# Performance work log

Hardware: AMD Instinct MI355X
Metric: run time of the kernel (lower is better)

Reference implementation:

```python
import jax, jax.numpy as jnp
import numpy as np

B, N, D, H = 2, 2048, 1024, 16
DH = D // H  # 64


def setup_inputs() -> dict:
    key = jax.random.key(0)
    ks = jax.random.split(key, 5)
    s = 1.0 / np.sqrt(D)
    x = jax.random.normal(ks[0], (B, N, D), jnp.float32)
    # per-head kqv Linear weights, stacked: [H, D, 3*DH]
    Wkqv = jax.random.normal(ks[1], (H, D, 3 * DH), jnp.float32) * s
    bkqv = jax.random.normal(ks[2], (H, 3 * DH), jnp.float32) * 0.02
    Wo = jax.random.normal(ks[3], (D, D), jnp.float32) * s
    bo = jax.random.normal(ks[4], (D,), jnp.float32) * 0.02
    return {"x": x, "Wkqv": Wkqv, "bkqv": bkqv, "Wo": Wo, "bo": bo}


def reference(x, Wkqv, bkqv, Wo, bo):
    Bs, Ns, Ds = x.shape
    Hs = Wkqv.shape[0]
    dh = Wkqv.shape[-1] // 3
    # all heads' kqv projections at once: [B, H, N, 3*dh]
    kqv_out = jnp.einsum('bnd,hde->bhne', x, Wkqv) + bkqv[None, :, None, :]
    # original splits in order (k, q, v)
    k, q, v = jnp.split(kqv_out, 3, axis=-1)
    # NOTE: original computes attention_scores(k, q) = k @ q^T (swapped vs standard)
    A = jnp.einsum('bhnd,bhmd->bhnm', k, q) / jnp.sqrt(jnp.asarray(dh, x.dtype))
    mask = jnp.tril(jnp.ones((Ns, Ns), dtype=bool))
    A = jnp.where(mask[None, None], A, -jnp.inf)
    alpha = jax.nn.softmax(A, axis=-1)
    sa = jnp.einsum('bhnm,bhmd->bhnd', alpha, v)  # [B, H, N, dh]
    # concat heads along feature dim (head0..headH-1 order)
    sa = sa.transpose(0, 2, 1, 3).reshape(Bs, Ns, Hs * dh)
    return sa @ Wo + bo
```

## Files before the change

### kernel.cpp

```cpp
#include <hip/hip_runtime.h>
#include <hip/hip_bf16.h>
#include <cstdint>
#include <cstddef>

typedef __bf16 bf16x8 __attribute__((ext_vector_type(8)));
typedef __bf16 bf16x4 __attribute__((ext_vector_type(4)));
typedef float  f32x4  __attribute__((ext_vector_type(4)));

constexpr int Bc = 2, Nc = 2048, Dc = 1024, Hc = 16, DHc = 64;
constexpr int BN = Bc * Nc;
constexpr int E3 = 3 * DHc;
constexpr int BH = Bc * Hc;
constexpr int NK = Hc * E3;

__device__ __forceinline__ f32x4 mfma16(bf16x8 a, bf16x8 b, f32x4 c) {
  return __builtin_amdgcn_mfma_f32_16x16x32_bf16(a, b, c, 0, 0, 0);
}

__device__ __forceinline__ void gload16(const __bf16* g, __bf16* l) {
  __builtin_amdgcn_global_load_lds((const __attribute__((address_space(1))) void*)g,
                                   (__attribute__((address_space(3))) void*)l,
                                   16, 0, 0);
}

__device__ __forceinline__ float fexp2(float x) {
  return __builtin_amdgcn_exp2f(x);
}

__global__ void cvt_x_kernel(const float* __restrict__ x, __bf16* __restrict__ xb) {
  int i = (blockIdx.x * 256 + threadIdx.x) * 4;
  float4 v = *(const float4*)(x + i);
  xb[i + 0] = (__bf16)v.x;
  xb[i + 1] = (__bf16)v.y;
  xb[i + 2] = (__bf16)v.z;
  xb[i + 3] = (__bf16)v.w;
}

constexpr int TP = 68;
__global__ void cvt_T_kernel(const float* __restrict__ src, __bf16* __restrict__ dst,
                             int R, int C) {
  __shared__ __bf16 T[64][TP];
  const int c0 = blockIdx.x * 64, r0 = blockIdx.y * 64;
  const size_t sbase = (size_t)blockIdx.z * R * C;
  const int tid = threadIdx.x;
#pragma unroll
  for (int it = 0; it < 4; ++it) {
    int g = tid + it * 256;
    int r = g >> 4, c4 = (g & 15) * 4;
    float4 v = *(const float4*)&src[sbase + (size_t)(r0 + r) * C + c0 + c4];
    T[c4 + 0][r] = (__bf16)v.x;
    T[c4 + 1][r] = (__bf16)v.y;
    T[c4 + 2][r] = (__bf16)v.z;
    T[c4 + 3][r] = (__bf16)v.w;
  }
  __syncthreads();
#pragma unroll
  for (int it = 0; it < 2; ++it) {
    int g = tid + it * 256;
    int c = g >> 3, ch = (g & 7) * 8;
    bf16x4 u0 = *(const bf16x4*)&T[c][ch];
    bf16x4 u1 = *(const bf16x4*)&T[c][ch + 4];
    __bf16* dp = &dst[sbase + (size_t)(c0 + c) * R + r0 + ch];
    *(bf16x4*)dp = u0;
    *(bf16x4*)(dp + 4) = u1;
  }
}

__launch_bounds__(256)
__global__ void kqv_gemm_kernel(const __bf16* __restrict__ xb,
                                const __bf16* __restrict__ wkt,
                                const float* __restrict__ bkqv,
                                __bf16* __restrict__ kqv,
                                __bf16* __restrict__ vT) {
  const int mt = blockIdx.x;
  const int h  = blockIdx.y;
  __shared__ __align__(16) __bf16 Al[2][128][64];
  __shared__ __align__(16) __bf16 Bl[2][192][64];
  const int tid  = threadIdx.x;
  const int lane = tid & 63;
  const int w    = tid >> 6;
  const int fr   = lane & 15, fq = lane >> 4;
  const int fq4  = fq * 4;
  const int WR   = (w >> 1) * 64, WC = (w & 1) * 96;
  const int sr   = tid >> 3;
  const int sc8  = ((tid & 7) ^ (sr & 7)) * 8;
  const int wb   = (w << 3);
  const int m0   = mt * 128;
  const __bf16* wth = wkt + (size_t)h * E3 * Dc;

  auto STAGE = [&](int buf, int k0) {
#pragma unroll
    for (int j = 0; j < 4; ++j)
      gload16(&xb[(size_t)(m0 + j * 32 + sr) * Dc + k0 + sc8], &Al[buf][j * 32 + wb][0]);
#pragma unroll
    for (int j = 0; j < 6; ++j)
      gload16(&wth[(size_t)(j * 32 + sr) * Dc + k0 + sc8], &Bl[buf][j * 32 + wb][0]);
  };

  f32x4 acc[4][6] = {};
  STAGE(0, 0);
  int cur = 0;
  for (int t = 0; t < 16; ++t) {
    if (t < 15) {
      STAGE(cur ^ 1, (t + 1) * 64);
      asm volatile("s_waitcnt vmcnt(10)" ::: "memory");
    } else {
      asm volatile("s_waitcnt vmcnt(0)" ::: "memory");
    }
    asm volatile("s_barrier" ::: "memory");
    const char* Ab = (const char*)&Al[cur][0][0];
    const char* Bb = (const char*)&Bl[cur][0][0];
#pragma unroll
    for (int ks = 0; ks < 2; ++ks) {
      bf16x8 a_[4], b_[6];
#pragma unroll
      for (int mr = 0; mr < 4; ++mr) {
        int r = WR + mr * 16 + fr;
        a_[mr] = *(const bf16x8*)(Ab + r * 128 + ((ks * 64 + fq * 16) ^ ((r & 7) << 4)));
      }
#pragma unroll
      for (int nc = 0; nc < 6; ++nc) {
        int r = WC + nc * 16 + fr;
        b_[nc] = *(const bf16x8*)(Bb + r * 128 + ((ks * 64 + fq * 16) ^ ((r & 7) << 4)));
      }
#pragma unroll
      for (int mr = 0; mr < 4; ++mr)
#pragma unroll
        for (int nc = 0; nc < 6; ++nc)
          acc[mr][nc] = mfma16(a_[mr], b_[nc], acc[mr][nc]);
    }
    asm volatile("s_barrier" ::: "memory");
    cur ^= 1;
  }

  const int b = m0 >> 11;
#pragma unroll
  for (int nc = 0; nc < 6; ++nc) {
    const int eb = WC + nc * 16;
    const float bias = bkqv[h * E3 + eb + fr];
    if (eb < 64) {
      const float sc = 0.125f * 1.44269504088896f;
      const int el = eb + fr;
#pragma unroll
      for (int mr = 0; mr < 4; ++mr) {
        int nn0 = (m0 & (Nc - 1)) + WR + mr * 16 + fq4;
        bf16x4 v4;
#pragma unroll
        for (int i = 0; i < 4; ++i) v4[i] = (__bf16)((acc[mr][nc][i] + bias) * sc);
        *(bf16x4*)&kqv[((size_t)((b * Hc + h) * DHc + el)) * Nc + nn0] = v4;
      }
    } else if (eb < 128) {
      const int e = (eb - 64) + fr;
      __bf16* dst = kqv + (size_t)BH * Nc * DHc +
                    ((size_t)(b * Hc + h)) * Nc * DHc + e;
#pragma unroll
      for (int mr = 0; mr < 4; ++mr)
#pragma unroll
        for (int i = 0; i < 4; ++i) {
          int n = (m0 & (Nc - 1)) + WR + mr * 16 + fq4 + i;
          dst[(size_t)n * DHc] = (__bf16)(acc[mr][nc][i] + bias);
        }
    } else {
      const int el = eb - 128 + fr;
#pragma unroll
      for (int mr = 0; mr < 4; ++mr) {
        int nn0 = (m0 & (Nc - 1)) + WR + mr * 16 + fq4;
        bf16x4 v4;
#pragma unroll
        for (int i = 0; i < 4; ++i) v4[i] = (__bf16)(acc[mr][nc][i] + bias);
        *(bf16x4*)&vT[((size_t)((b * Hc + h) * DHc + el)) * Nc + nn0] = v4;
      }
    }
  }
}

__launch_bounds__(256)
__global__ void attn_kernel(const __bf16* __restrict__ kT,
                            const __bf16* __restrict__ qb,
                            const __bf16* __restrict__ vT,
                            __bf16* __restrict__ sab) {
  const int bx = blockIdx.x;
  const int by = blockIdx.y;
  const int bh   = 4 * (bx & 7) + (by >> 3);
  const int pair = (bx >> 3) * 8 + (by & 7);
  __shared__ __align__(16) __bf16 KqL[2][64][64];
  __shared__ __align__(16) __bf16 VtL[2][64][64];
  __shared__ __align__(16) __bf16 Pl[4][16][64];
  const int tid  = threadIdx.x;
  const int lane = tid & 63;
  const int w    = tid >> 6;
  const int fr   = lane & 15, fq = lane >> 4;
  const int fq4  = fq * 4;
  const int key  = (fr & 7) << 4;
  const int off0 = (fq * 16) ^ key;
  const int off1 = (fq * 16 + 64) ^ key;
  const __bf16* kth = kT + (size_t)bh * DHc * Nc;
  const __bf16* qbh = qb + (size_t)bh * Nc * DHc;
  const __bf16* vth = vT + (size_t)bh * DHc * Nc;
  const int b = bh >> 4, h = bh & 15;
  char* Pw = (char*)&Pl[w][0][0];

  const int sch  = (tid & 7);
  const int r_s0 = tid >> 3;
  const int r_s1 = r_s0 + 32;
  const int swb0 = r_s0 * 128 + ((sch * 16) ^ ((r_s0 & 7) << 4));
  const int swb1 = r_s1 * 128 + ((sch * 16) ^ ((r_s1 & 7) << 4));

  for (int ph = 0; ph < 2; ++ph) {
    const int qt   = ph ? (31 - pair) : pair;
    const int n0   = qt * 64 + w * 16;
    const int ncol = n0 + fr;

    bf16x8 bq0, bq1;
#pragma unroll
    for (int j = 0; j < 8; ++j) {
      bq0[j] = kth[(size_t)(8 * fq + j) * Nc + n0 + fr];
      bq1[j] = kth[(size_t)(32 + 8 * fq + j) * Nc + n0 + fr];
    }

    float l_run = 0.f;
    f32x4 acc[4] = {};

    __syncthreads();
    {
      bf16x8 k0a = *(const bf16x8*)&qbh[(size_t)r_s0 * DHc + sch * 8];
      bf16x8 k0b = *(const bf16x8*)&qbh[(size_t)r_s1 * DHc + sch * 8];
      bf16x8 v0a = *(const bf16x8*)&vth[(size_t)r_s0 * Nc + sch * 8];
      bf16x8 v0b = *(const bf16x8*)&vth[(size_t)r_s1 * Nc + sch * 8];
      *(bf16x8*)((char*)&KqL[0][0][0] + swb0) = k0a;
      *(bf16x8*)((char*)&KqL[0][0][0] + swb1) = k0b;
      *(bf16x8*)((char*)&VtL[0][0][0] + swb0) = v0a;
      *(bf16x8*)((char*)&VtL[0][0][0] + swb1) = v0b;
    }
    __syncthreads();

    int cur = 0;
    for (int t = 0; t <= qt; ++t) {
      bf16x8 nk0, nk1, nv0, nv1;
      const bool more = (t < qt);
      if (more) {
        const int v1 = (t + 1) * 64;
        nk0 = *(const bf16x8*)&qbh[(size_t)(v1 + r_s0) * DHc + sch * 8];
        nk1 = *(const bf16x8*)&qbh[(size_t)(v1 + r_s1) * DHc + sch * 8];
        nv0 = *(const bf16x8*)&vth[(size_t)r_s0 * Nc + v1 + sch * 8];
        nv1 = *(const bf16x8*)&vth[(size_t)r_s1 * Nc + v1 + sch * 8];
      }

      const char* Kqb = (const char*)&KqL[cur][0][0];
      const char* Vtb = (const char*)&VtL[cur][0][0];

      f32x4 s[4];
      __builtin_amdgcn_s_setprio(1);
#pragma unroll
      for (int c = 0; c < 4; ++c) {
        const char* rp = Kqb + (c * 16 + fr) * 128;
        bf16x8 t0 = *(const bf16x8*)(rp + off0);
        bf16x8 t1 = *(const bf16x8*)(rp + off1);
        f32x4 z = {};
        z = mfma16(t0, bq0, z);
        z = mfma16(t1, bq1, z);
        s[c] = z;
      }
      __builtin_amdgcn_s_setprio(0);

      if (t == qt) {
        const int thr = ncol - t * 64;
#pragma unroll
        for (int c = 0; c < 4; ++c)
#pragma unroll
          for (int i = 0; i < 4; ++i) {
            float pv = fexp2(s[c][i]);
            s[c][i] = (c * 16 + fq4 + i > thr) ? 0.f : pv;
          }
      } else {
#pragma unroll
        for (int c = 0; c < 4; ++c)
#pragma unroll
          for (int i = 0; i < 4; ++i) s[c][i] = fexp2(s[c][i]);
      }
      float cs0 = (s[0][0] + s[0][1]) + (s[0][2] + s[0][3]);
      float cs1 = (s[1][0] + s[1][1]) + (s[1][2] + s[1][3]);
      float cs2 = (s[2][0] + s[2][1]) + (s[2][2] + s[2][3]);
      float cs3 = (s[3][0] + s[3][1]) + (s[3][2] + s[3][3]);
      l_run += (cs0 + cs1) + (cs2 + cs3);

#pragma unroll
      for (int c = 0; c < 4; ++c) {
        bf16x4 p4;
#pragma unroll
        for (int i = 0; i < 4; ++i) p4[i] = (__bf16)s[c][i];
        *(bf16x4*)(Pw + fr * 128 + ((c * 32 + fq * 8) ^ key)) = p4;
      }
      asm volatile("s_waitcnt lgkmcnt(0)" ::: "memory");
      __builtin_amdgcn_sched_barrier(0);

      __builtin_amdgcn_s_setprio(1);
      bf16x8 ap0 = *(const bf16x8*)(Pw + fr * 128 + off0);
      bf16x8 ap1 = *(const bf16x8*)(Pw + fr * 128 + off1);
#pragma unroll
      for (int d = 0; d < 4; ++d) {
        const char* vp = Vtb + (d * 16 + fr) * 128;
        bf16x8 bv0 = *(const bf16x8*)(vp + off0);
        bf16x8 bv1 = *(const bf16x8*)(vp + off1);
        acc[d] = mfma16(ap0, bv0, acc[d]);
        acc[d] = mfma16(ap1, bv1, acc[d]);
      }
      __builtin_amdgcn_s_setprio(0);

      if (more) {
        char* Kn = (char*)&KqL[cur ^ 1][0][0];
        char* Vn = (char*)&VtL[cur ^ 1][0][0];
        *(bf16x8*)(Kn + swb0) = nk0;
        *(bf16x8*)(Kn + swb1) = nk1;
        *(bf16x8*)(Vn + swb0) = nv0;
        *(bf16x8*)(Vn + swb1) = nv1;
      }
      __syncthreads();
      cur ^= 1;
    }

    l_run += __shfl_xor(l_run, 16);
    l_run += __shfl_xor(l_run, 32);
    float linv[4];
#pragma unroll
    for (int ii = 0; ii < 4; ++ii) linv[ii] = 1.0f / __shfl(l_run, fq4 + ii);
#pragma unroll
    for (int d = 0; d < 4; ++d)
#pragma unroll
      for (int ii = 0; ii < 4; ++ii) {
        int n  = n0 + fq4 + ii;
        int dd = d * 16 + fr;
        sab[((size_t)(b * Nc + n)) * Dc + h * DHc + dd] = (__bf16)(acc[d][ii] * linv[ii]);
      }
  }
}

__launch_bounds__(256)
__global__ void out_gemm_kernel(const __bf16* __restrict__ sab,
                                const __bf16* __restrict__ wot,
                                const float* __restrict__ bo,
                                float* __restrict__ out) {
  const int mt = blockIdx.x;
  const int nt = blockIdx.y;
  __shared__ __align__(16) __bf16 Al[2][128][64];
  __shared__ __align__(16) __bf16 Bl[2][128][64];
  const int tid  = threadIdx.x;
  const int lane = tid & 63;
  const int w    = tid >> 6;
  const int fr   = lane & 15, fq = lane >> 4;
  const int fq4  = fq * 4;
  const int WR   = (w >> 1) * 64, WC = (w & 1) * 64;
  const int sr   = tid >> 3;
  const int sc8  = ((tid & 7) ^ (sr & 7)) * 8;
  const int wb   = (w << 3);
  const int m0   = mt * 128, n0 = nt * 128;

  auto STAGE = [&](int buf, int k0) {
#pragma unroll
    for (int j = 0; j < 4; ++j)
      gload16(&sab[(size_t)(m0 + j * 32 + sr) * Dc + k0 + sc8], &Al[buf][j * 32 + wb][0]);
#pragma unroll
    for (int j = 0; j < 4; ++j)
      gload16(&wot[(size_t)(n0 + j * 32 + sr) * Dc + k0 + sc8], &Bl[buf][j * 32 + wb][0]);
  };

  f32x4 acc[4][4] = {};
  STAGE(0, 0);
  int cur = 0;
  for (int t = 0; t < 16; ++t) {
    if (t < 15) {
      STAGE(cur ^ 1, (t + 1) * 64);
      asm volatile("s_waitcnt vmcnt(8)" ::: "memory");
    } else {
      asm volatile("s_waitcnt vmcnt(0)" ::: "memory");
    }
    asm volatile("s_barrier" ::: "memory");
    const char* Ab = (const char*)&Al[cur][0][0];
    const char* Bb = (const char*)&Bl[cur][0][0];
#pragma unroll
    for (int ks = 0; ks < 2; ++ks) {
      bf16x8 a_[4], b_[4];
#pragma unroll
      for (int mr = 0; mr < 4; ++mr) {
        int r = WR + mr * 16 + fr;
        a_[mr] = *(const bf16x8*)(Ab + r * 128 + ((ks * 64 + fq * 16) ^ ((r & 7) << 4)));
      }
#pragma unroll
      for (int nc = 0; nc < 4; ++nc) {
        int r = WC + nc * 16 + fr;
        b_[nc] = *(const bf16x8*)(Bb + r * 128 + ((ks * 64 + fq * 16) ^ ((r & 7) << 4)));
      }
#pragma unroll
      for (int mr = 0; mr < 4; ++mr)
#pragma unroll
        for (int nc = 0; nc < 4; ++nc)
          acc[mr][nc] = mfma16(a_[mr], b_[nc], acc[mr][nc]);
    }
    asm volatile("s_barrier" ::: "memory");
    cur ^= 1;
  }
#pragma unroll
  for (int mr = 0; mr < 4; ++mr)
#pragma unroll
    for (int nc = 0; nc < 4; ++nc)
#pragma unroll
      for (int i = 0; i < 4; ++i) {
        int m = m0 + WR + mr * 16 + fq4 + i;
        int e = n0 + WC + nc * 16 + fr;
        out[(size_t)m * Dc + e] = acc[mr][nc][i] + bo[e];
      }
}

extern "C" void kernel_launch(void* const* d_in, const int* in_sizes, int n_in,
                              void* d_out, int out_size, void* d_ws, size_t ws_size,
                              hipStream_t stream) {
  const float* x    = (const float*)d_in[0];
  const float* Wkqv = (const float*)d_in[1];
  const float* bkqv = (const float*)d_in[2];
  const float* Wo   = (const float*)d_in[3];
  const float* bo   = (const float*)d_in[4];
  float* out = (float*)d_out;

  __bf16* xb   = (__bf16*)d_ws;
  __bf16* wkt  = xb  + (size_t)BN * Dc;
  __bf16* wot  = wkt + (size_t)NK * Dc;
  __bf16* kqv  = wot + (size_t)Dc * Dc;
  __bf16* kTb  = kqv;
  __bf16* qbuf = kqv + (size_t)BH * Nc * DHc;
  __bf16* vTb  = kqv + 2 * (size_t)BH * Nc * DHc;
  __bf16* sab  = kqv + 3 * (size_t)BH * Nc * DHc;

  cvt_x_kernel<<<(BN * Dc) / (256 * 4), 256, 0, stream>>>(x, xb);
  cvt_T_kernel<<<dim3(E3 / 64, Dc / 64, Hc), 256, 0, stream>>>(Wkqv, wkt, Dc, E3);
  cvt_T_kernel<<<dim3(Dc / 64, Dc / 64, 1), 256, 0, stream>>>(Wo, wot, Dc, Dc);

  kqv_gemm_kernel<<<dim3(BN / 128, Hc), 256, 0, stream>>>(xb, wkt, bkqv, kqv, vTb);

  attn_kernel<<<dim3(16, BH), 256, 0, stream>>>(kTb, qbuf, vTb, sab);

  out_gemm_kernel<<<dim3(BN / 128, Dc / 128), 256, 0, stream>>>(sab, wot, bo, out);
}
```

Baseline: 102.0 us.

## Stage K/V tiles with direct global-to-LDS loads and vmcnt-based double buffering

Replaces register-staged prefetch of the key and value tiles (global load into registers, then LDS store after compute) with direct global_load_lds transfers into the alternate LDS buffer. Waits use s_waitcnt vmcnt counts plus raw barriers. The swizzle moves from the LDS destination address to the global source column. This removes register pressure and the explicit LDS store instructions from the attention loop and lets the copy overlap compute. The trade-off is reliance on hand-written waitcnt/barrier correctness for the asynchronous LDS writes.

```diff
diff --git a/kernel.cpp b/kernel.cpp
--- a/kernel.cpp
+++ b/kernel.cpp
@@ -200,11 +200,8 @@
   const int b = bh >> 4, h = bh & 15;
   char* Pw = (char*)&Pl[w][0][0];
 
-  const int sch  = (tid & 7);
-  const int r_s0 = tid >> 3;
-  const int r_s1 = r_s0 + 32;
-  const int swb0 = r_s0 * 128 + ((sch * 16) ^ ((r_s0 & 7) << 4));
-  const int swb1 = r_s1 * 128 + ((sch * 16) ^ ((r_s1 & 7) << 4));
+  const int srow = lane >> 3;
+  const int sc8  = ((lane & 7) ^ srow) * 8;
 
   for (int ph = 0; ph < 2; ++ph) {
     const int qt   = ph ? (31 - pair) : pair;
@@ -221,30 +218,27 @@
     float l_run = 0.f;
     f32x4 acc[4] = {};
 
+    auto STAGE = [&](int buf, int t) {
+      const int v0 = t * 64;
+#pragma unroll
+      for (int j = 0; j < 2; ++j) {
+        const int r = w * 16 + j * 8;
+        gload16(&qbh[(size_t)(v0 + r + srow) * DHc + sc8], &KqL[buf][r][0]);
+        gload16(&vth[(size_t)(r + srow) * Nc + v0 + sc8], &VtL[buf][r][0]);
+      }
+    };
+
     __syncthreads();
-    {
-      bf16x8 k0a = *(const bf16x8*)&qbh[(size_t)r_s0 * DHc + sch * 8];
-      bf16x8 k0b = *(const bf16x8*)&qbh[(size_t)r_s1 * DHc + sch * 8];
-      bf16x8 v0a = *(const bf16x8*)&vth[(size_t)r_s0 * Nc + sch * 8];
-      bf16x8 v0b = *(const bf16x8*)&vth[(size_t)r_s1 * Nc + sch * 8];
-      *(bf16x8*)((char*)&KqL[0][0][0] + swb0) = k0a;
-      *(bf16x8*)((char*)&KqL[0][0][0] + swb1) = k0b;
-      *(bf16x8*)((char*)&VtL[0][0][0] + swb0) = v0a;
-      *(bf16x8*)((char*)&VtL[0][0][0] + swb1) = v0b;
-    }
-    __syncthreads();
-
+    STAGE(0, 0);
     int cur = 0;
     for (int t = 0; t <= qt; ++t) {
-      bf16x8 nk0, nk1, nv0, nv1;
-      const bool more = (t < qt);
-      if (more) {
-        const int v1 = (t + 1) * 64;
-        nk0 = *(const bf16x8*)&qbh[(size_t)(v1 + r_s0) * DHc + sch * 8];
-        nk1 = *(const bf16x8*)&qbh[(size_t)(v1 + r_s1) * DHc + sch * 8];
-        nv0 = *(const bf16x8*)&vth[(size_t)r_s0 * Nc + v1 + sch * 8];
-        nv1 = *(const bf16x8*)&vth[(size_t)r_s1 * Nc + v1 + sch * 8];
-      }
+      if (t < qt) {
+        STAGE(cur ^ 1, t + 1);
+        asm volatile("s_waitcnt vmcnt(4)" ::: "memory");
+      } else {
+        asm volatile("s_waitcnt vmcnt(0)" ::: "memory");
+      }
+      asm volatile("s_barrier" ::: "memory");
 
       const char* Kqb = (const char*)&KqL[cur][0][0];
       const char* Vtb = (const char*)&VtL[cur][0][0];
@@ -306,16 +300,7 @@
         acc[d] = mfma16(ap1, bv1, acc[d]);
       }
       __builtin_amdgcn_s_setprio(0);
-
-      if (more) {
-        char* Kn = (char*)&KqL[cur ^ 1][0][0];
-        char* Vn = (char*)&VtL[cur ^ 1][0][0];
-        *(bf16x8*)(Kn + swb0) = nk0;
-        *(bf16x8*)(Kn + swb1) = nk1;
-        *(bf16x8*)(Vn + swb0) = nv0;
-        *(bf16x8*)(Vn + swb1) = nv1;
-      }
-      __syncthreads();
+      asm volatile("s_barrier" ::: "memory");
       cur ^= 1;
     }
 
```

Result: slower. 105.4 us (+3.3%).
